# Optimization experiments

Hardware: AMD Instinct MI355X
Metric: run time of the kernel (lower is better)

The kernel has to match this reference:

```python
import jax, jax.numpy as jnp
import numpy as np

N = 100000
E = 3200000
IN_DIM = 256
HID = 128
OUT_DIM = 64


def setup_inputs() -> dict:
    key = jax.random.key(0)
    ks = jax.random.split(key, 8)
    features = jax.random.normal(ks[0], (N, IN_DIM), dtype=jnp.float32)
    edge_row = jax.random.randint(ks[1], (E,), 0, N, dtype=jnp.int32)
    edge_col = jax.random.randint(ks[2], (E,), 0, N, dtype=jnp.int32)
    edge_val = jax.random.uniform(ks[3], (E,), dtype=jnp.float32)
    W1 = jax.random.normal(ks[4], (IN_DIM, HID), dtype=jnp.float32) * (1.0 / np.sqrt(IN_DIM))
    b1 = jnp.zeros((HID,), dtype=jnp.float32)
    W2 = jax.random.normal(ks[5], (HID, OUT_DIM), dtype=jnp.float32) * (1.0 / np.sqrt(HID))
    b2 = jnp.zeros((OUT_DIM,), dtype=jnp.float32)
    return {"features": features, "edge_row": edge_row, "edge_col": edge_col,
            "edge_val": edge_val, "W1": W1, "b1": b1, "W2": W2, "b2": b2}


def reference(features, edge_row, edge_col, edge_val, W1, b1, W2, b2):
    # fc1: [N, IN_DIM] @ [IN_DIM, HID] + b1
    h = features @ W1 + b1                                   # [N, HID]
    # spmm(A, h): for each edge (r, c, v): out[r] += v * h[c]
    msgs = edge_val[:, None] * h[edge_col]                    # [E, HID] gather
    h = jax.ops.segment_sum(msgs, edge_row, num_segments=N)   # [N, HID] scatter-add
    h = jax.nn.relu(h)
    h = h @ W2 + b2                                           # [N, OUT_DIM]
    return jax.nn.log_softmax(h, axis=1)
```

## Files before the change

kernel.cpp:

```cpp
#include <hip/hip_runtime.h>
#include <math.h>

constexpr int IN_DIM  = 256;
constexpr int HID     = 128;
constexpr int OUT_DIM = 64;

constexpr int BROWS   = 128;
constexpr int NBUCK   = 782;
constexpr int CAP     = 4608;
constexpr int CAP2    = 5504;
constexpr int CHUNK   = 8192;
constexpr int GC_STRIDE = 16;

typedef short  bf16x8 __attribute__((ext_vector_type(8)));
typedef float  f32x4  __attribute__((ext_vector_type(4)));
typedef float  f32x2  __attribute__((ext_vector_type(2)));
typedef int    i32x4  __attribute__((ext_vector_type(4)));

__device__ __forceinline__ unsigned short f2bf(float x) {
    union { float f; unsigned u; } v; v.f = x;
    unsigned r = v.u + 0x7FFF + ((v.u >> 16) & 1);
    return (unsigned short)(r >> 16);
}

__global__ __launch_bounds__(256) void wt_kernel(const float* __restrict__ W1,
                                                 const float* __restrict__ W2,
                                                 unsigned short* __restrict__ W1T,
                                                 unsigned short* __restrict__ W2T)
{
    int idx = blockIdx.x * 256 + threadIdx.x;
    if (idx < IN_DIM * HID) {
        int k = idx >> 7;
        int n = idx & 127;
        W1T[n * IN_DIM + k] = f2bf(W1[idx]);
    } else {
        int j = idx - IN_DIM * HID;
        int k = j >> 6;
        int n = j & 63;
        W2T[n * HID + k] = f2bf(W2[j]);
    }
}

__global__ __launch_bounds__(256) void fc1_mfma(const float* __restrict__ feat,
                                                const unsigned short* __restrict__ W1T,
                                                const float* __restrict__ b1,
                                                unsigned short* __restrict__ h1b, int N)
{
    const int t    = threadIdx.x;
    const int lane = t & 63;
    const int w    = t >> 6;
    const int quad = lane >> 4;
    const int ln15 = lane & 15;
    const int row0 = blockIdx.x * 64;

    int arow = row0 + w * 16 + ln15;
    if (arow >= N) arow = N - 1;
    const float* aptr = feat + (size_t)arow * IN_DIM + quad * 8;

    f32x4 acc[8];
#pragma unroll
    for (int i = 0; i < 8; ++i) acc[i] = (f32x4){0.f, 0.f, 0.f, 0.f};

#pragma unroll
    for (int ks = 0; ks < 8; ++ks) {
        float4 a0 = *(const float4*)(aptr + ks * 32);
        float4 a1 = *(const float4*)(aptr + ks * 32 + 4);
        bf16x8 afrag;
        afrag[0] = (short)f2bf(a0.x); afrag[1] = (short)f2bf(a0.y);
        afrag[2] = (short)f2bf(a0.z); afrag[3] = (short)f2bf(a0.w);
        afrag[4] = (short)f2bf(a1.x); afrag[5] = (short)f2bf(a1.y);
        afrag[6] = (short)f2bf(a1.z); afrag[7] = (short)f2bf(a1.w);
#pragma unroll
        for (int nt = 0; nt < 8; ++nt) {
            bf16x8 bfrag = *(const bf16x8*)&W1T[(size_t)(nt * 16 + ln15) * IN_DIM + ks * 32 + quad * 8];
            acc[nt] = __builtin_amdgcn_mfma_f32_16x16x32_bf16(afrag, bfrag, acc[nt], 0, 0, 0);
        }
    }

#pragma unroll
    for (int nt = 0; nt < 8; ++nt) {
        int col = nt * 16 + ln15;
        float bias = b1[col];
#pragma unroll
        for (int r = 0; r < 4; ++r) {
            int grow = row0 + w * 16 + quad * 4 + r;
            if (grow < N)
                h1b[(size_t)grow * HID + col] = f2bf(acc[nt][r] + bias);
        }
    }
}

__global__ __launch_bounds__(1024) void bin_kernel(const int* __restrict__ erow,
                                                   const int* __restrict__ ecol,
                                                   const float* __restrict__ eval,
                                                   int* __restrict__ gCursor,
                                                   int2* __restrict__ binned, int E)
{
    __shared__ int sCnt[NBUCK];
    __shared__ int sBase[NBUCK];
    const int t = threadIdx.x;
    const int e0 = blockIdx.x * CHUNK;
    const int eEnd = min(e0 + CHUNK, E);

    for (int i = t; i < NBUCK; i += 1024) sCnt[i] = 0;
    __syncthreads();

    for (int e = e0 + t; e < eEnd; e += 1024)
        atomicAdd(&sCnt[erow[e] >> 7], 1);
    __syncthreads();

    for (int i = t; i < NBUCK; i += 1024) {
        int c = sCnt[i];
        sBase[i] = c ? atomicAdd(&gCursor[i * GC_STRIDE], c) : 0;
        sCnt[i] = 0;
    }
    __syncthreads();

    for (int e = e0 + t; e < eEnd; e += 1024) {
        int   r = erow[e];
        int   c = ecol[e];
        float v = eval[e];
        int   b = r >> 7;
        int off = sBase[b] + atomicAdd(&sCnt[b], 1);
        if (off < CAP)
            binned[(size_t)b * CAP + off] = make_int2((c << 8) | ((r & 127) << 25),
                                                      __float_as_int(v));
    }
}

__global__ __launch_bounds__(256) void sort_bucket4(const int* __restrict__ gCursor,
                                                    const int2* __restrict__ binned,
                                                    int2* __restrict__ edges2,
                                                    int2* __restrict__ rowIdx, int N)
{
    __shared__ int2 sE[CAP];
    __shared__ int sHist[BROWS];
    __shared__ int sStart[BROWS + 1];
    __shared__ int sCur[BROWS];
    const int t  = threadIdx.x;
    const int b  = blockIdx.x;
    const int nE = min(gCursor[b * GC_STRIDE], CAP);
    const size_t baseIn  = (size_t)b * CAP;
    const size_t baseOut = (size_t)b * CAP2;

    if (t < BROWS) sHist[t] = 0;
    __syncthreads();

    for (int i = t; i < nE; i += 256) {
        int2 p = binned[baseIn + i];
        sE[i] = p;
        atomicAdd(&sHist[(unsigned)p.x >> 25], 1);
    }
    __syncthreads();

    if (t < BROWS) sStart[t + 1] = (sHist[t] + 7) & ~7;
    if (t == 0) sStart[0] = 0;
    __syncthreads();
    for (int o = 1; o < BROWS; o <<= 1) {
        int v = 0;
        if (t < BROWS) {
            v = sStart[t + 1];
            if (t >= o) v += sStart[t + 1 - o];
        }
        __syncthreads();
        if (t < BROWS) sStart[t + 1] = v;
        __syncthreads();
    }
    if (t < BROWS) sCur[t] = sStart[t];
    __syncthreads();

    for (int i = t; i < nE; i += 256) {
        int2 p = sE[i];
        int rl = (unsigned)p.x >> 25;
        int pos = atomicAdd(&sCur[rl], 1);
        edges2[baseOut + pos] = p;
    }

    if (t < BROWS) {
        int h  = sHist[t];
        int ph = (h + 7) & ~7;
        size_t p0 = baseOut + sStart[t];
        for (int k = h; k < ph; ++k)
            edges2[p0 + k] = make_int2(0, 0);
        int rr = b * BROWS + t;
        if (rr < N)
            rowIdx[rr] = make_int2((int)p0, (int)(p0 + ph));
    }
}

__global__ __launch_bounds__(256) void spmm_kernel(const int2* __restrict__ rowIdx,
                                                   const int2* __restrict__ edges2,
                                                   const unsigned short* __restrict__ h1b,
                                                   unsigned* __restrict__ h2b, int N)
{
    const int lane  = threadIdx.x & 63;
    const int lane4 = lane * 4;
    const int r     = (blockIdx.x * blockDim.x + threadIdx.x) >> 6;
    if (r >= N) return;
    const char* h1base = (const char*)h1b;

    const int2 se = rowIdx[r];
    int j = se.x;
    const int jend = se.y;
    f32x2 acc = (f32x2){0.f, 0.f};

    for (; j + 16 <= jend; j += 16) {
        i32x4 q[8];
#pragma unroll
        for (int u = 0; u < 8; ++u)
            q[u] = __builtin_nontemporal_load((const i32x4*)&edges2[j + u * 2]);
        unsigned g[16];
#pragma unroll
        for (int u = 0; u < 8; ++u) {
            g[2 * u]     = *(const unsigned*)(h1base + (q[u].x & 0x01FFFFFF) + lane4);
            g[2 * u + 1] = *(const unsigned*)(h1base + (q[u].z & 0x01FFFFFF) + lane4);
        }
#pragma unroll
        for (int u = 0; u < 8; ++u) {
            f32x2 h0 = (f32x2){__uint_as_float(g[2 * u] << 16),
                               __uint_as_float(g[2 * u] & 0xFFFF0000u)};
            f32x2 h1 = (f32x2){__uint_as_float(g[2 * u + 1] << 16),
                               __uint_as_float(g[2 * u + 1] & 0xFFFF0000u)};
            acc += h0 * __int_as_float(q[u].y);
            acc += h1 * __int_as_float(q[u].w);
        }
    }
    if (j < jend) {
        i32x4 q[4];
#pragma unroll
        for (int u = 0; u < 4; ++u)
            q[u] = __builtin_nontemporal_load((const i32x4*)&edges2[j + u * 2]);
        unsigned g[8];
#pragma unroll
        for (int u = 0; u < 4; ++u) {
            g[2 * u]     = *(const unsigned*)(h1base + (q[u].x & 0x01FFFFFF) + lane4);
            g[2 * u + 1] = *(const unsigned*)(h1base + (q[u].z & 0x01FFFFFF) + lane4);
        }
#pragma unroll
        for (int u = 0; u < 4; ++u) {
            f32x2 h0 = (f32x2){__uint_as_float(g[2 * u] << 16),
                               __uint_as_float(g[2 * u] & 0xFFFF0000u)};
            f32x2 h1 = (f32x2){__uint_as_float(g[2 * u + 1] << 16),
                               __uint_as_float(g[2 * u + 1] & 0xFFFF0000u)};
            acc += h0 * __int_as_float(q[u].y);
            acc += h1 * __int_as_float(q[u].w);
        }
    }

    float ax = fmaxf(acc.x, 0.f), ay = fmaxf(acc.y, 0.f);
    h2b[(size_t)r * 64 + lane] = (unsigned)f2bf(ax) | ((unsigned)f2bf(ay) << 16);
}

__global__ __launch_bounds__(256) void fc2_mfma(const unsigned short* __restrict__ h2b,
                                                const unsigned short* __restrict__ W2T,
                                                const float* __restrict__ b2,
                                                float* __restrict__ out, int N)
{
    const int t    = threadIdx.x;
    const int lane = t & 63;
    const int w    = t >> 6;
    const int quad = lane >> 4;
    const int ln15 = lane & 15;
    const int row0 = blockIdx.x * 64;

    int arow = row0 + w * 16 + ln15;
    if (arow >= N) arow = N - 1;

    f32x4 acc[4];
#pragma unroll
    for (int i = 0; i < 4; ++i) acc[i] = (f32x4){0.f, 0.f, 0.f, 0.f};

#pragma unroll
    for (int ks = 0; ks < 4; ++ks) {
        bf16x8 afrag = *(const bf16x8*)&h2b[(size_t)arow * HID + ks * 32 + quad * 8];
#pragma unroll
        for (int nt = 0; nt < 4; ++nt) {
            bf16x8 bfrag = *(const bf16x8*)&W2T[(size_t)(nt * 16 + ln15) * HID + ks * 32 + quad * 8];
            acc[nt] = __builtin_amdgcn_mfma_f32_16x16x32_bf16(afrag, bfrag, acc[nt], 0, 0, 0);
        }
    }

    float bias[4];
#pragma unroll
    for (int nt = 0; nt < 4; ++nt) bias[nt] = b2[nt * 16 + ln15];

#pragma unroll
    for (int r = 0; r < 4; ++r) {
        float v[4];
#pragma unroll
        for (int nt = 0; nt < 4; ++nt) v[nt] = acc[nt][r] + bias[nt];

        float m = fmaxf(fmaxf(v[0], v[1]), fmaxf(v[2], v[3]));
#pragma unroll
        for (int o = 1; o < 16; o <<= 1) m = fmaxf(m, __shfl_xor(m, o));
        float s = __expf(v[0] - m) + __expf(v[1] - m) +
                  __expf(v[2] - m) + __expf(v[3] - m);
#pragma unroll
        for (int o = 1; o < 16; o <<= 1) s += __shfl_xor(s, o);
        float ls = __logf(s);

        int grow = row0 + w * 16 + quad * 4 + r;
        if (grow < N) {
#pragma unroll
            for (int nt = 0; nt < 4; ++nt)
                out[(size_t)grow * OUT_DIM + nt * 16 + ln15] = v[nt] - m - ls;
        }
    }
}

extern "C" void kernel_launch(void* const* d_in, const int* in_sizes, int n_in,
                              void* d_out, int out_size, void* d_ws, size_t ws_size,
                              hipStream_t stream) {
    const float* feat = (const float*)d_in[0];
    const int*   erow = (const int*)d_in[1];
    const int*   ecol = (const int*)d_in[2];
    const float* eval = (const float*)d_in[3];
    const float* W1   = (const float*)d_in[4];
    const float* b1   = (const float*)d_in[5];
    const float* W2   = (const float*)d_in[6];
    const float* b2   = (const float*)d_in[7];
    float*       out  = (float*)d_out;

    const int N = in_sizes[0] / IN_DIM;
    const int E = in_sizes[1];

    unsigned short* h1b    = (unsigned short*)d_ws;
    unsigned short* h2b    = h1b + (size_t)N * HID;
    int2*           binned = (int2*)(h2b + (size_t)N * HID);
    int2*           edges2 = binned + (size_t)NBUCK * CAP;
    int2*           rowIdx = edges2 + (size_t)NBUCK * CAP2;
    unsigned short* W1T    = (unsigned short*)(rowIdx + N);
    unsigned short* W2T    = W1T + IN_DIM * HID;
    int*            gCursor= (int*)(W2T + HID * OUT_DIM);

    hipMemsetAsync(gCursor, 0, NBUCK * GC_STRIDE * sizeof(int), stream);

    wt_kernel<<<(IN_DIM * HID + HID * OUT_DIM) / 256, 256, 0, stream>>>(W1, W2, W1T, W2T);
    fc1_mfma<<<(N + 63) / 64, 256, 0, stream>>>(feat, W1T, b1, h1b, N);
    bin_kernel<<<(E + CHUNK - 1) / CHUNK, 1024, 0, stream>>>(erow, ecol, eval,
                                                             gCursor, binned, E);
    sort_bucket4<<<NBUCK, 256, 0, stream>>>(gCursor, binned, edges2, rowIdx, N);

    const int nblk = (N + 3) / 4;
    spmm_kernel<<<nblk, 256, 0, stream>>>(rowIdx, edges2, h1b,
                                          (unsigned*)h2b, N);
    fc2_mfma<<<(N + 63) / 64, 256, 0, stream>>>(h2b, W2T, b2, out, N);
}
```

Before: 469.4 us.

## Stage fc1 feature tiles via global_load_lds and split SpMM into two launches

fc1 now copies each 64-row feature tile into padded LDS with direct global-to-LDS 16-byte loads, then reads A fragments from LDS instead of doing strided global float4 loads. The SpMM launch is split into two half-range launches over rows. The LDS staging is meant to coalesce the feature reads, at the cost of 66KB of shared memory per block, which lowers occupancy. The split launch adds launch overhead and has no obvious benefit, unless it is meant to improve cache locality or to probe timing.

```diff
diff --git a/kernel.cpp b/kernel.cpp
--- a/kernel.cpp
+++ b/kernel.cpp
@@ -21,6 +21,12 @@
     union { float f; unsigned u; } v; v.f = x;
     unsigned r = v.u + 0x7FFF + ((v.u >> 16) & 1);
     return (unsigned short)(r >> 16);
+}
+
+__device__ __forceinline__ void load_lds16(const void* g, void* l) {
+    __builtin_amdgcn_global_load_lds(
+        (const __attribute__((address_space(1))) unsigned int*)g,
+        (__attribute__((address_space(3))) unsigned int*)l, 16, 0, 0);
 }
 
 __global__ __launch_bounds__(256) void wt_kernel(const float* __restrict__ W1,
@@ -41,11 +47,14 @@
     }
 }
 
+constexpr int FPAD = 260;
+
 __global__ __launch_bounds__(256) void fc1_mfma(const float* __restrict__ feat,
                                                 const unsigned short* __restrict__ W1T,
                                                 const float* __restrict__ b1,
                                                 unsigned short* __restrict__ h1b, int N)
 {
+    __shared__ float sF[64 * FPAD];
     const int t    = threadIdx.x;
     const int lane = t & 63;
     const int w    = t >> 6;
@@ -53,9 +62,16 @@
     const int ln15 = lane & 15;
     const int row0 = blockIdx.x * 64;
 
-    int arow = row0 + w * 16 + ln15;
-    if (arow >= N) arow = N - 1;
-    const float* aptr = feat + (size_t)arow * IN_DIM + quad * 8;
+#pragma unroll
+    for (int i = 0; i < 16; ++i) {
+        int r  = w * 16 + i;
+        int gr = row0 + r;
+        if (gr < N)
+            load_lds16(feat + (size_t)gr * IN_DIM + lane * 4, &sF[r * FPAD]);
+    }
+    __syncthreads();
+
+    const float* aptr = &sF[(w * 16 + ln15) * FPAD + quad * 8];
 
     f32x4 acc[8];
 #pragma unroll
@@ -191,12 +207,13 @@
 __global__ __launch_bounds__(256) void spmm_kernel(const int2* __restrict__ rowIdx,
                                                    const int2* __restrict__ edges2,
                                                    const unsigned short* __restrict__ h1b,
-                                                   unsigned* __restrict__ h2b, int N)
+                                                   unsigned* __restrict__ h2b,
+                                                   int rbase, int rend)
 {
     const int lane  = threadIdx.x & 63;
     const int lane4 = lane * 4;
-    const int r     = (blockIdx.x * blockDim.x + threadIdx.x) >> 6;
-    if (r >= N) return;
+    const int r     = rbase + ((blockIdx.x * blockDim.x + threadIdx.x) >> 6);
+    if (r >= rend) return;
     const char* h1base = (const char*)h1b;
 
     const int2 se = rowIdx[r];
@@ -341,8 +358,10 @@
                                                              gCursor, binned, E);
     sort_bucket4<<<NBUCK, 256, 0, stream>>>(gCursor, binned, edges2, rowIdx, N);
 
-    const int nblk = (N + 3) / 4;
-    spmm_kernel<<<nblk, 256, 0, stream>>>(rowIdx, edges2, h1b,
-                                          (unsigned*)h2b, N);
+    const int half = ((N + 1) / 2 + 3) & ~3;
+    spmm_kernel<<<half / 4, 256, 0, stream>>>(rowIdx, edges2, h1b,
+                                              (unsigned*)h2b, 0, half);
+    spmm_kernel<<<(N - half + 3) / 4, 256, 0, stream>>>(rowIdx, edges2, h1b,
+                                                        (unsigned*)h2b, half, N);
     fc2_mfma<<<(N + 63) / 64, 256, 0, stream>>>(h2b, W2T, b2, out, N);
 }
```

Result: slower. 485.8 us (+3.5%).
